# Optimization experiments

Measured on AMD Instinct MI355X. Metric: run time of the kernel, lower is better.

The kernel has to match this reference:

```python
import jax, jax.numpy as jnp
import numpy as np

N_NODES = 50000
N_FEAT = 256
N_HID = 256
N_CLASS = 40
N_EDGES = 800000


def setup_inputs() -> dict:
    key = jax.random.key(0)
    ks = jax.random.split(key, 12)
    x = jax.random.normal(ks[0], (N_NODES, N_FEAT), dtype=jnp.float32)
    edge_index = jax.random.randint(ks[1], (2, N_EDGES), 0, N_NODES, dtype=jnp.int64)
    def glorot(k, fan_in, fan_out):
        s = jnp.sqrt(6.0 / (fan_in + fan_out)).astype(jnp.float32)
        return jax.random.uniform(k, (fan_in, fan_out), jnp.float32, -s, s)
    return {
        "x": x,
        "edge_index": edge_index,
        "W1": glorot(ks[2], N_FEAT, N_HID), "b1": jnp.zeros((N_HID,), jnp.float32),
        "W2": glorot(ks[3], N_HID, N_HID), "b2": jnp.zeros((N_HID,), jnp.float32),
        "W3": glorot(ks[4], N_HID, N_HID), "b3": jnp.zeros((N_HID,), jnp.float32),
        "W4": glorot(ks[5], N_HID, N_CLASS), "b4": jnp.zeros((N_CLASS,), jnp.float32),
    }


def _gcn_norm(edge_index, num_nodes):
    # add self-loops, compute symmetric normalization (PyG gcn_norm)
    loop = jnp.arange(num_nodes, dtype=edge_index.dtype)
    src = jnp.concatenate([edge_index[0], loop])
    dst = jnp.concatenate([edge_index[1], loop])
    deg = jax.ops.segment_sum(jnp.ones_like(dst, dtype=jnp.float32), dst,
                              num_segments=num_nodes)
    dis = jnp.where(deg > 0, jax.lax.rsqrt(deg), 0.0)
    norm = dis[src] * dis[dst]  # [E + N]
    return src, dst, norm


def _gcn_conv(x, W, b, src, dst, norm, num_nodes):
    h = x @ W  # dense transform first (out_channels <= in_channels)
    msg = norm[:, None] * h[src]  # gather + scale
    out = jax.ops.segment_sum(msg, dst, num_segments=num_nodes)  # scatter-add
    return out + b


def reference(x, edge_index, W1, b1, W2, b2, W3, b3, W4, b4):
    n = x.shape[0]
    src, dst, norm = _gcn_norm(edge_index, n)
    h = jax.nn.relu(_gcn_conv(x, W1, b1, src, dst, norm, n))
    # dropout is identity in eval mode
    h = jax.nn.relu(_gcn_conv(h, W2, b2, src, dst, norm, n))
    h = jax.nn.relu(_gcn_conv(h, W3, b3, src, dst, norm, n))
    out = _gcn_conv(h, W4, b4, src, dst, norm, n)
    return out
```

## Files before the change

### kernel.cpp

```cpp
#include <hip/hip_runtime.h>

#define NN 50000
#define NF 256
#define NH 256
#define NC 40
#define NE 800000

typedef _Float16 f16x8 __attribute__((ext_vector_type(8)));
typedef float f32x4 __attribute__((ext_vector_type(4)));

__device__ __forceinline__ float f16f(unsigned short u) {
  union { unsigned short u; _Float16 h; } a; a.u = u;
  return (float)a.h;
}
__device__ __forceinline__ unsigned short f16u(float f) {
  union { unsigned short u; _Float16 h; } a; a.h = (_Float16)f;
  return a.u;
}

__device__ __forceinline__ void gl16(const void* g, void* l) {
  __builtin_amdgcn_global_load_lds(
      (const __attribute__((address_space(1))) unsigned int*)g,
      (__attribute__((address_space(3))) unsigned int*)l, 16, 0, 0);
}


__global__ void count_kernel(const int* __restrict__ dst, int* __restrict__ cnt) {
  int e = blockIdx.x * blockDim.x + threadIdx.x;
  if (e < NE) atomicAdd(&cnt[dst[e]], 1);
}

__global__ __launch_bounds__(1024) void scan1_kernel(const int* __restrict__ cnt,
                                                     int* __restrict__ row_ptr,
                                                     int* __restrict__ bsum,
                                                     float* __restrict__ dis) {
  __shared__ int s[1024];
  int i = blockIdx.x * 1024 + threadIdx.x;
  int v = (i < NN) ? cnt[i] : 0;
  if (i < NN) dis[i] = rsqrtf((float)(v + 1));
  s[threadIdx.x] = v;
  __syncthreads();
  for (int ofs = 1; ofs < 1024; ofs <<= 1) {
    int t = (threadIdx.x >= ofs) ? s[threadIdx.x - ofs] : 0;
    __syncthreads();
    s[threadIdx.x] += t;
    __syncthreads();
  }
  if (i < NN) row_ptr[i] = s[threadIdx.x] - v;
  if (threadIdx.x == 1023) bsum[blockIdx.x] = s[1023];
}

__global__ __launch_bounds__(1024) void scan23_kernel(int* __restrict__ row_ptr,
                                                      const int* __restrict__ bsum) {
  __shared__ int sb[64];
  const int nb = (NN + 1023) / 1024;
  if (threadIdx.x < 64) {
    int lane = threadIdx.x;
    int v = (lane < nb) ? bsum[lane] : 0;
    for (int ofs = 1; ofs < 64; ofs <<= 1) {
      int t = __shfl_up(v, ofs, 64);
      if (lane >= ofs) v += t;
    }
    sb[lane] = v;
  }
  __syncthreads();
  int i = blockIdx.x * 1024 + threadIdx.x;
  int add = (blockIdx.x > 0) ? sb[blockIdx.x - 1] : 0;
  if (i < NN) row_ptr[i] += add;
  if (i == 0) row_ptr[NN] = NE;
}

__global__ void scatter_kernel(const int* __restrict__ src, const int* __restrict__ dst,
                               const int* __restrict__ row_ptr, int* __restrict__ cur,
                               int2* __restrict__ ew, const float* __restrict__ dis) {
  int e = blockIdx.x * blockDim.x + threadIdx.x;
  if (e < NE) {
    int d = dst[e], s = src[e];
    int pos = row_ptr[d] + atomicAdd(&cur[d], 1);
    int2 v; v.x = s; v.y = __float_as_int(dis[s] * dis[d]);
    ew[pos] = v;
  }
}


__global__ void wf16_kernel(const float* __restrict__ W1, const float* __restrict__ W2,
                            const float* __restrict__ W3, const float* __restrict__ W4,
                            unsigned short* __restrict__ Wt1, unsigned short* __restrict__ Wt2,
                            unsigned short* __restrict__ Wt3, unsigned short* __restrict__ Wt4) {
  int idx = blockIdx.x * blockDim.x + threadIdx.x;
  const float* W; unsigned short* Wt; int N;
  if (idx < 65536)       { W = W1; Wt = Wt1; N = 256; }
  else if (idx < 131072) { W = W2; Wt = Wt2; N = 256; idx -= 65536; }
  else if (idx < 196608) { W = W3; Wt = Wt3; N = 256; idx -= 131072; }
  else if (idx < 229376) { W = W4; Wt = Wt4; N = 40;  idx -= 196608; }
  else return;
  int n = idx >> 8, k = idx & 255;
  float v = (n < N) ? W[k * N + n] : 0.0f;
  Wt[idx] = f16u(v);
}


template <int NSTORE, bool AF32>
__global__ __launch_bounds__(256, 2) void gemm_f16(
    const void* __restrict__ Ain, const unsigned short* __restrict__ Bt,
    unsigned short* __restrict__ Cout, int M) {
  __shared__ unsigned short lds[2][2][128 * 64];

  int tid = threadIdx.x;
  int rowBase = blockIdx.x * 128;
  int colBase = blockIdx.y * 128;
  int w = tid >> 6, lane = tid & 63;
  int wr = w >> 1, wc = w & 1;
  int l15 = lane & 15, l4 = lane >> 4;

  f32x4 acc[4][4] = {};

  auto stage = [&](int kt, int buf) {
#pragma unroll
    for (int c = 0; c < 4; ++c) {
      int gi = c * 256 + tid;
      int row = gi >> 3, gp = gi & 7;
      int gsrc = gp ^ (row & 7);
      int koff = kt * 64 + gsrc * 8;
      int ar = rowBase + row; ar = ar < M ? ar : M - 1;
      if (AF32) {
        const float* Af = (const float*)Ain + (size_t)ar * 256 + koff;
        float4 v0 = *(const float4*)Af;
        float4 v1 = *(const float4*)(Af + 4);
        f16x8 h = {(_Float16)v0.x, (_Float16)v0.y, (_Float16)v0.z, (_Float16)v0.w,
                   (_Float16)v1.x, (_Float16)v1.y, (_Float16)v1.z, (_Float16)v1.w};
        *(f16x8*)&lds[buf][0][gi * 8] = h;
      } else {
        gl16((const unsigned short*)Ain + (size_t)ar * 256 + koff, &lds[buf][0][gi * 8]);
      }
      int br = colBase + row;
      gl16(Bt + (size_t)br * 256 + koff, &lds[buf][1][gi * 8]);
    }
  };

  stage(0, 0);
  __syncthreads();

  for (int kt = 0; kt < 4; ++kt) {
    int buf = kt & 1;
    if (kt < 3) stage(kt + 1, buf ^ 1);

#pragma unroll
    for (int ks = 0; ks < 2; ++ks) {
      f16x8 a[4], b[4];
      int g = ks * 4 + l4;
#pragma unroll
      for (int mi = 0; mi < 4; ++mi) {
        int row = wr * 64 + mi * 16 + l15;
        int gp = g ^ (row & 7);
        a[mi] = *(const f16x8*)&lds[buf][0][row * 64 + gp * 8];
      }
#pragma unroll
      for (int ni = 0; ni < 4; ++ni) {
        int row = wc * 64 + ni * 16 + l15;
        int gp = g ^ (row & 7);
        b[ni] = *(const f16x8*)&lds[buf][1][row * 64 + gp * 8];
      }
#pragma unroll
      for (int mi = 0; mi < 4; ++mi)
#pragma unroll
        for (int ni = 0; ni < 4; ++ni)
          acc[mi][ni] = __builtin_amdgcn_mfma_f32_16x16x32_f16(a[mi], b[ni], acc[mi][ni], 0, 0, 0);
    }
    __syncthreads();
  }

#pragma unroll
  for (int ni = 0; ni < 4; ++ni) {
    int col = colBase + wc * 64 + ni * 16 + l15;
    if (col < NSTORE) {
#pragma unroll
      for (int mi = 0; mi < 4; ++mi) {
        f32x4 v = acc[mi][ni];
#pragma unroll
        for (int i = 0; i < 4; ++i) {
          int r = rowBase + wr * 64 + mi * 16 + l4 * 4 + i;
          if (r < M) Cout[(size_t)r * NSTORE + col] = f16u(v[i]);
        }
      }
    }
  }
}


__global__ __launch_bounds__(256) void agg256_kernel(
    const unsigned short* __restrict__ T, unsigned short* __restrict__ P,
    const int* __restrict__ rp, const int2* __restrict__ ew,
    const float* __restrict__ dis, const float* __restrict__ b) {
  int node = (blockIdx.x * blockDim.x + threadIdx.x) >> 6;
  int lane = threadIdx.x & 63;
  if (node >= NN) return;
  const ushort4* Tv = (const ushort4*)T;
  float4 bv = ((const float4*)b)[lane];
  float d = dis[node];
  float w0 = d * d;
  ushort4 t = Tv[(size_t)node * 64 + lane];
  float ax = bv.x + w0 * f16f(t.x), ay = bv.y + w0 * f16f(t.y);
  float az = bv.z + w0 * f16f(t.z), aw = bv.w + w0 * f16f(t.w);
  int e = rp[node], end = rp[node + 1];
  for (; e + 4 <= end; e += 4) {
    int2 e0 = ew[e], e1 = ew[e + 1], e2 = ew[e + 2], e3 = ew[e + 3];
    ushort4 t0 = Tv[(size_t)e0.x * 64 + lane];
    ushort4 t1 = Tv[(size_t)e1.x * 64 + lane];
    ushort4 t2 = Tv[(size_t)e2.x * 64 + lane];
    ushort4 t3 = Tv[(size_t)e3.x * 64 + lane];
    float f0 = __int_as_float(e0.y), f1 = __int_as_float(e1.y);
    float f2 = __int_as_float(e2.y), f3 = __int_as_float(e3.y);
    ax += f0 * f16f(t0.x) + f1 * f16f(t1.x) + f2 * f16f(t2.x) + f3 * f16f(t3.x);
    ay += f0 * f16f(t0.y) + f1 * f16f(t1.y) + f2 * f16f(t2.y) + f3 * f16f(t3.y);
    az += f0 * f16f(t0.z) + f1 * f16f(t1.z) + f2 * f16f(t2.z) + f3 * f16f(t3.z);
    aw += f0 * f16f(t0.w) + f1 * f16f(t1.w) + f2 * f16f(t2.w) + f3 * f16f(t3.w);
  }
  for (; e < end; ++e) {
    int2 sw = ew[e];
    float f = __int_as_float(sw.y);
    ushort4 ts = Tv[(size_t)sw.x * 64 + lane];
    ax += f * f16f(ts.x); ay += f * f16f(ts.y);
    az += f * f16f(ts.z); aw += f * f16f(ts.w);
  }
  ax = fmaxf(ax, 0.f); ay = fmaxf(ay, 0.f);
  az = fmaxf(az, 0.f); aw = fmaxf(aw, 0.f);
  ushort4 h;
  h.x = f16u(ax); h.y = f16u(ay); h.z = f16u(az); h.w = f16u(aw);
  ((ushort4*)P)[(size_t)node * 64 + lane] = h;
}

__global__ __launch_bounds__(256) void agg40_kernel(
    const unsigned short* __restrict__ T, float* __restrict__ O,
    const int* __restrict__ rp, const int2* __restrict__ ew,
    const float* __restrict__ dis, const float* __restrict__ b) {
  int node = (blockIdx.x * blockDim.x + threadIdx.x) >> 6;
  int lane = threadIdx.x & 63;
  if (node >= NN) return;
  float d = dis[node];
  int e = rp[node], end = rp[node + 1];
  if (lane < NC) {
    float acc = b[lane] + d * d * f16f(T[(size_t)node * NC + lane]);
    for (; e + 4 <= end; e += 4) {
      int2 e0 = ew[e], e1 = ew[e + 1], e2 = ew[e + 2], e3 = ew[e + 3];
      float t0 = f16f(T[(size_t)e0.x * NC + lane]);
      float t1 = f16f(T[(size_t)e1.x * NC + lane]);
      float t2 = f16f(T[(size_t)e2.x * NC + lane]);
      float t3 = f16f(T[(size_t)e3.x * NC + lane]);
      acc += __int_as_float(e0.y) * t0 + __int_as_float(e1.y) * t1 +
             __int_as_float(e2.y) * t2 + __int_as_float(e3.y) * t3;
    }
    for (; e < end; ++e) {
      int2 sw = ew[e];
      acc += __int_as_float(sw.y) * f16f(T[(size_t)sw.x * NC + lane]);
    }
    O[(size_t)node * NC + lane] = acc;
  }
}


extern "C" void kernel_launch(void* const* d_in, const int* in_sizes, int n_in,
                              void* d_out, int out_size, void* d_ws, size_t ws_size,
                              hipStream_t stream) {
  const float* x  = (const float*)d_in[0];
  const int* edge = (const int*)d_in[1];
  const float* W1 = (const float*)d_in[2];
  const float* b1 = (const float*)d_in[3];
  const float* W2 = (const float*)d_in[4];
  const float* b2 = (const float*)d_in[5];
  const float* W3 = (const float*)d_in[6];
  const float* b3 = (const float*)d_in[7];
  const float* W4 = (const float*)d_in[8];
  const float* b4 = (const float*)d_in[9];
  float* out = (float*)d_out;

  char* p = (char*)d_ws;
  unsigned short* T16 = (unsigned short*)p; p += (size_t)NN * NH * 2;
  unsigned short* P16 = (unsigned short*)p; p += (size_t)NN * NH * 2;
  int* cnt = (int*)p;                p += (size_t)NN * 4;
  int* cur = (int*)p;                p += (size_t)NN * 4;
  float* dis = (float*)p;            p += (size_t)NN * 4;
  int* row_ptr = (int*)p;            p += (size_t)(NN + 16) * 4;
  int* bsum = (int*)p;               p += 256 * 4;
  int2* ew = (int2*)p;               p += (size_t)NE * 8;
  unsigned short* Wt1 = (unsigned short*)p; p += 256 * 256 * 2;
  unsigned short* Wt2 = (unsigned short*)p; p += 256 * 256 * 2;
  unsigned short* Wt3 = (unsigned short*)p; p += 256 * 256 * 2;
  unsigned short* Wt4 = (unsigned short*)p; p += 128 * 256 * 2;

  const int* e_src = edge;
  const int* e_dst = edge + NE;

  hipMemsetAsync(cnt, 0, (size_t)NN * 8, stream);

  const int nb1024 = (NN + 1023) / 1024;
  count_kernel<<<(NE + 255) / 256, 256, 0, stream>>>(e_dst, cnt);
  scan1_kernel<<<nb1024, 1024, 0, stream>>>(cnt, row_ptr, bsum, dis);
  scan23_kernel<<<nb1024, 1024, 0, stream>>>(row_ptr, bsum);
  scatter_kernel<<<(NE + 255) / 256, 256, 0, stream>>>(e_src, e_dst, row_ptr, cur, ew, dis);

  wf16_kernel<<<(229376 + 255) / 256, 256, 0, stream>>>(W1, W2, W3, W4, Wt1, Wt2, Wt3, Wt4);

  dim3 gFull((NN + 127) / 128, 2);
  dim3 gLast((NN + 127) / 128, 1);
  int aggBlocks = (NN * 64 + 255) / 256;

  gemm_f16<256, true><<<gFull, 256, 0, stream>>>(x, Wt1, T16, NN);
  agg256_kernel<<<aggBlocks, 256, 0, stream>>>(T16, P16, row_ptr, ew, dis, b1);
  gemm_f16<256, false><<<gFull, 256, 0, stream>>>(P16, Wt2, T16, NN);
  agg256_kernel<<<aggBlocks, 256, 0, stream>>>(T16, P16, row_ptr, ew, dis, b2);
  gemm_f16<256, false><<<gFull, 256, 0, stream>>>(P16, Wt3, T16, NN);
  agg256_kernel<<<aggBlocks, 256, 0, stream>>>(T16, P16, row_ptr, ew, dis, b3);
  gemm_f16<NC, false><<<gLast, 256, 0, stream>>>(P16, Wt4, T16, NN);
  agg40_kernel<<<aggBlocks, 256, 0, stream>>>(T16, out, row_ptr, ew, dis, b4);
}
```

Baseline: 378.7 us.

## Retile GEMM to 64x256 full-width blocks without double buffering

The GEMM now gives each block 64 rows and all 256 output columns (one 64-column slice per wave), so the A tile is read once per row block instead of once per column-block grid half. Double buffering is dropped for a single stage-then-sync loop, LDS use per block shrinks, and launch bounds move to 4 blocks per CU. The last layer stores a padded 64-wide output, and agg40 reads with a stride of 64. The cost is no overlap between loads and MFMA inside a block, plus extra padded work and storage for the 40-class layer.

After: 380.2 us. About the same (+0.4%).

```diff
diff --git a/kernel.cpp b/kernel.cpp
--- a/kernel.cpp
+++ b/kernel.cpp
@@ -92,7 +92,7 @@
   if (idx < 65536)       { W = W1; Wt = Wt1; N = 256; }
   else if (idx < 131072) { W = W2; Wt = Wt2; N = 256; idx -= 65536; }
   else if (idx < 196608) { W = W3; Wt = Wt3; N = 256; idx -= 131072; }
-  else if (idx < 229376) { W = W4; Wt = Wt4; N = 40;  idx -= 196608; }
+  else if (idx < 262144) { W = W4; Wt = Wt4; N = 40;  idx -= 196608; }
   else return;
   int n = idx >> 8, k = idx & 255;
   float v = (n < N) ? W[k * N + n] : 0.0f;
@@ -101,23 +101,22 @@
 
 
 template <int NSTORE, bool AF32>
-__global__ __launch_bounds__(256, 2) void gemm_f16(
+__global__ __launch_bounds__(256, 4) void gemm_f16(
     const void* __restrict__ Ain, const unsigned short* __restrict__ Bt,
     unsigned short* __restrict__ Cout, int M) {
-  __shared__ unsigned short lds[2][2][128 * 64];
+  __shared__ unsigned short ldsA[64 * 64];
+  __shared__ unsigned short ldsB[256 * 64];
 
   int tid = threadIdx.x;
-  int rowBase = blockIdx.x * 128;
-  int colBase = blockIdx.y * 128;
+  int rowBase = blockIdx.x * 64;
   int w = tid >> 6, lane = tid & 63;
-  int wr = w >> 1, wc = w & 1;
   int l15 = lane & 15, l4 = lane >> 4;
 
   f32x4 acc[4][4] = {};
 
-  auto stage = [&](int kt, int buf) {
-#pragma unroll
-    for (int c = 0; c < 4; ++c) {
+  for (int kt = 0; kt < 4; ++kt) {
+#pragma unroll
+    for (int c = 0; c < 2; ++c) {
       int gi = c * 256 + tid;
       int row = gi >> 3, gp = gi & 7;
       int gsrc = gp ^ (row & 7);
@@ -129,21 +128,20 @@
         float4 v1 = *(const float4*)(Af + 4);
         f16x8 h = {(_Float16)v0.x, (_Float16)v0.y, (_Float16)v0.z, (_Float16)v0.w,
                    (_Float16)v1.x, (_Float16)v1.y, (_Float16)v1.z, (_Float16)v1.w};
-        *(f16x8*)&lds[buf][0][gi * 8] = h;
+        *(f16x8*)&ldsA[gi * 8] = h;
       } else {
-        gl16((const unsigned short*)Ain + (size_t)ar * 256 + koff, &lds[buf][0][gi * 8]);
+        gl16((const unsigned short*)Ain + (size_t)ar * 256 + koff, &ldsA[gi * 8]);
       }
-      int br = colBase + row;
-      gl16(Bt + (size_t)br * 256 + koff, &lds[buf][1][gi * 8]);
-    }
-  };
-
-  stage(0, 0);
-  __syncthreads();
-
-  for (int kt = 0; kt < 4; ++kt) {
-    int buf = kt & 1;
-    if (kt < 3) stage(kt + 1, buf ^ 1);
+    }
+#pragma unroll
+    for (int c = 0; c < 8; ++c) {
+      int gi = c * 256 + tid;
+      int row = gi >> 3, gp = gi & 7;
+      int gsrc = gp ^ (row & 7);
+      int koff = kt * 64 + gsrc * 8;
+      gl16(Bt + (size_t)row * 256 + koff, &ldsB[gi * 8]);
+    }
+    __syncthreads();
 
 #pragma unroll
     for (int ks = 0; ks < 2; ++ks) {
@@ -151,15 +149,15 @@
       int g = ks * 4 + l4;
 #pragma unroll
       for (int mi = 0; mi < 4; ++mi) {
-        int row = wr * 64 + mi * 16 + l15;
-        int gp = g ^ (row & 7);
-        a[mi] = *(const f16x8*)&lds[buf][0][row * 64 + gp * 8];
+        int arow = mi * 16 + l15;
+        int gp = g ^ (arow & 7);
+        a[mi] = *(const f16x8*)&ldsA[arow * 64 + gp * 8];
       }
 #pragma unroll
       for (int ni = 0; ni < 4; ++ni) {
-        int row = wc * 64 + ni * 16 + l15;
-        int gp = g ^ (row & 7);
-        b[ni] = *(const f16x8*)&lds[buf][1][row * 64 + gp * 8];
+        int brow = w * 64 + ni * 16 + l15;
+        int gp = g ^ (brow & 7);
+        b[ni] = *(const f16x8*)&ldsB[brow * 64 + gp * 8];
       }
 #pragma unroll
       for (int mi = 0; mi < 4; ++mi)
@@ -172,14 +170,14 @@
 
 #pragma unroll
   for (int ni = 0; ni < 4; ++ni) {
-    int col = colBase + wc * 64 + ni * 16 + l15;
+    int col = w * 64 + ni * 16 + l15;
     if (col < NSTORE) {
 #pragma unroll
       for (int mi = 0; mi < 4; ++mi) {
         f32x4 v = acc[mi][ni];
 #pragma unroll
         for (int i = 0; i < 4; ++i) {
-          int r = rowBase + wr * 64 + mi * 16 + l4 * 4 + i;
+          int r = rowBase + mi * 16 + l4 * 4 + i;
           if (r < M) Cout[(size_t)r * NSTORE + col] = f16u(v[i]);
         }
       }
@@ -240,19 +238,19 @@
   float d = dis[node];
   int e = rp[node], end = rp[node + 1];
   if (lane < NC) {
-    float acc = b[lane] + d * d * f16f(T[(size_t)node * NC + lane]);
+    float acc = b[lane] + d * d * f16f(T[(size_t)node * 64 + lane]);
     for (; e + 4 <= end; e += 4) {
       int2 e0 = ew[e], e1 = ew[e + 1], e2 = ew[e + 2], e3 = ew[e + 3];
-      float t0 = f16f(T[(size_t)e0.x * NC + lane]);
-      float t1 = f16f(T[(size_t)e1.x * NC + lane]);
-      float t2 = f16f(T[(size_t)e2.x * NC + lane]);
-      float t3 = f16f(T[(size_t)e3.x * NC + lane]);
+      float t0 = f16f(T[(size_t)e0.x * 64 + lane]);
+      float t1 = f16f(T[(size_t)e1.x * 64 + lane]);
+      float t2 = f16f(T[(size_t)e2.x * 64 + lane]);
+      float t3 = f16f(T[(size_t)e3.x * 64 + lane]);
       acc += __int_as_float(e0.y) * t0 + __int_as_float(e1.y) * t1 +
              __int_as_float(e2.y) * t2 + __int_as_float(e3.y) * t3;
     }
     for (; e < end; ++e) {
       int2 sw = ew[e];
-      acc += __int_as_float(sw.y) * f16f(T[(size_t)sw.x * NC + lane]);
+      acc += __int_as_float(sw.y) * f16f(T[(size_t)sw.x * 64 + lane]);
     }
     O[(size_t)node * NC + lane] = acc;
   }
@@ -286,7 +284,7 @@
   unsigned short* Wt1 = (unsigned short*)p; p += 256 * 256 * 2;
   unsigned short* Wt2 = (unsigned short*)p; p += 256 * 256 * 2;
   unsigned short* Wt3 = (unsigned short*)p; p += 256 * 256 * 2;
-  unsigned short* Wt4 = (unsigned short*)p; p += 128 * 256 * 2;
+  unsigned short* Wt4 = (unsigned short*)p; p += 256 * 256 * 2;
 
   const int* e_src = edge;
   const int* e_dst = edge + NE;
@@ -299,18 +297,17 @@
   scan23_kernel<<<nb1024, 1024, 0, stream>>>(row_ptr, bsum);
   scatter_kernel<<<(NE + 255) / 256, 256, 0, stream>>>(e_src, e_dst, row_ptr, cur, ew, dis);
 
-  wf16_kernel<<<(229376 + 255) / 256, 256, 0, stream>>>(W1, W2, W3, W4, Wt1, Wt2, Wt3, Wt4);
-
-  dim3 gFull((NN + 127) / 128, 2);
-  dim3 gLast((NN + 127) / 128, 1);
+  wf16_kernel<<<(262144 + 255) / 256, 256, 0, stream>>>(W1, W2, W3, W4, Wt1, Wt2, Wt3, Wt4);
+
+  int gemmBlocks = (NN + 63) / 64;
   int aggBlocks = (NN * 64 + 255) / 256;
 
-  gemm_f16<256, true><<<gFull, 256, 0, stream>>>(x, Wt1, T16, NN);
+  gemm_f16<256, true><<<gemmBlocks, 256, 0, stream>>>(x, Wt1, T16, NN);
   agg256_kernel<<<aggBlocks, 256, 0, stream>>>(T16, P16, row_ptr, ew, dis, b1);
-  gemm_f16<256, false><<<gFull, 256, 0, stream>>>(P16, Wt2, T16, NN);
+  gemm_f16<256, false><<<gemmBlocks, 256, 0, stream>>>(P16, Wt2, T16, NN);
   agg256_kernel<<<aggBlocks, 256, 0, stream>>>(T16, P16, row_ptr, ew, dis, b2);
-  gemm_f16<256, false><<<gFull, 256, 0, stream>>>(P16, Wt3, T16, NN);
+  gemm_f16<256, false><<<gemmBlocks, 256, 0, stream>>>(P16, Wt3, T16, NN);
   agg256_kernel<<<aggBlocks, 256, 0, stream>>>(T16, P16, row_ptr, ew, dis, b3);
-  gemm_f16<NC, false><<<gLast, 256, 0, stream>>>(P16, Wt4, T16, NN);
+  gemm_f16<64, false><<<gemmBlocks, 256, 0, stream>>>(P16, Wt4, T16, NN);
   agg40_kernel<<<aggBlocks, 256, 0, stream>>>(T16, out, row_ptr, ew, dis, b4);
 }
```
